# Optimization experiments

Hardware: AMD Instinct MI355X
Metric: run time of the kernel (lower is better)

Reference implementation:

```python
import jax, jax.numpy as jnp
import numpy as np

B, L, D, H = 8, 512, 1024, 16
HD = D // H  # head dim = 64
SCALE = 1.0  # scale=False in __init__


def _rel_sinusoid(seq_len, dim):
    # RelativeSinusoidalPositionalEmbedding lookup for relative positions
    # arange(-L/2, L/2) (even L), sinusoid of the raw relative position.
    half = dim // 2
    inv = jnp.exp(jnp.arange(half, dtype=jnp.float32) * (-(np.log(10000.0) / (half - 1))))
    r = jnp.arange(-(seq_len // 2), seq_len // 2, dtype=jnp.float32)  # (L,)
    ang = r[:, None] * inv[None, :]  # (L, half)
    return jnp.concatenate([jnp.sin(ang), jnp.cos(ang)], axis=1)  # (L, dim)


def setup_inputs() -> dict:
    key = jax.random.key(0)
    ks = jax.random.split(key, 8)
    s = 0.02
    x = jax.random.normal(ks[0], (B, L, D), jnp.float32)
    mask = jax.random.randint(ks[1], (B, L), 0, 2).astype(jnp.int64)
    mask = mask.at[:, 0].set(1)  # ensure at least one valid key per row
    qmask = jax.random.randint(ks[2], (B, L), 0, 2).astype(jnp.int64)
    w_qkv = jax.random.normal(ks[3], (D, 3 * D), jnp.float32) * s
    w_qkpos = jax.random.normal(ks[4], (HD, 2 * D), jnp.float32) * s
    w_fc = jax.random.normal(ks[5], (D, D), jnp.float32) * s
    b_fc = jnp.zeros((D,), jnp.float32)
    shift = jnp.abs(jax.random.normal(ks[6], (1,), jnp.float32)) + 0.001
    bias = -jnp.abs(jax.random.normal(ks[7], (1,), jnp.float32))
    return dict(x=x, mask=mask, qmask=qmask, w_qkv=w_qkv, w_qkpos=w_qkpos,
                w_fc=w_fc, b_fc=b_fc, shift=shift, bias=bias)


def reference(x, mask, qmask, w_qkv, w_qkpos, w_fc, b_fc, shift, bias):
    # trans_type='self', use_Gaussian=True, dropout in eval mode (identity)
    b, l, d = x.shape
    qkv = x @ w_qkv  # (B, L, 3D)
    q, k, v = jnp.split(qkv, 3, axis=-1)
    q = q.reshape(b, l, H, HD).transpose(0, 2, 1, 3)  # (B,H,L,hd)
    k = k.reshape(b, l, H, HD).transpose(0, 2, 1, 3)
    v = v.reshape(b, l, H, HD).transpose(0, 2, 1, 3)

    pe = _rel_sinusoid(l, HD)               # (L, hd)
    y = pe @ w_qkpos                        # (L, 2D)
    q_p, k_p = jnp.split(y, 2, axis=-1)     # (L, D) each
    q_p = q_p.reshape(l, H, HD).transpose(1, 0, 2)  # (H, L, hd)
    k_p = k_p.reshape(l, H, HD).transpose(1, 0, 2)  # (H, L, hd)

    attn = jnp.einsum('bhid,bhjd->bhij', q, k) + jnp.einsum('hid,hjd->hij', q_p, k_p)[None]

    # speaker-identity masking: zero out cross-speaker scores (trans_type='self')
    qsame = qmask[:, :, None] == qmask[:, None, :]  # (B, L, L)
    attn = jnp.where(qsame[:, None], attn, 0.0)
    attn = attn / SCALE

    # key padding mask -> -inf
    attn = jnp.where(mask[:, None, None, :] == 0, -jnp.inf, attn)

    # Gaussian distance bias: -(shift * (i-j)^2 + bias)
    idx = jnp.arange(l, dtype=jnp.float32)
    sqd = (idx[:, None] - idx[None, :]) ** 2  # (L, L)
    attn = attn + (-(shift[0] * sqd + bias[0]))[None, None]

    attn = jax.nn.softmax(attn, axis=-1)
    out = jnp.einsum('bhij,bhjd->bhid', attn, v)  # (B,H,L,hd)
    out = out.transpose(0, 2, 1, 3).reshape(b, l, d)
    return out @ w_fc + b_fc
```

## Files before the change

kernel.cpp:

```cpp
#include <hip/hip_runtime.h>
#include <hip/hip_bf16.h>

#define BB 8
#define LL 512
#define DD 1024
#define HH 16
#define HD 64
#define LOG2E 1.4426950408889634f

typedef __attribute__((ext_vector_type(8))) unsigned short u16x8;
typedef __attribute__((ext_vector_type(4))) unsigned short u16x4;
typedef __attribute__((ext_vector_type(8))) __bf16 bf16x8;
typedef __attribute__((ext_vector_type(4))) float f32x4;
typedef __attribute__((ext_vector_type(16))) float f32x16;

#define DEV __device__ __forceinline__

DEV unsigned short f2bf(float f) {
    return __builtin_bit_cast(unsigned short, (__bf16)f);
}
DEV f32x4 mfma16(u16x8 a, u16x8 b, f32x4 c) {
    return __builtin_amdgcn_mfma_f32_16x16x32_bf16(
        __builtin_bit_cast(bf16x8, a), __builtin_bit_cast(bf16x8, b), c, 0, 0, 0);
}
DEV f32x16 mfma32(u16x8 a, u16x8 b, f32x16 c) {
    return __builtin_amdgcn_mfma_f32_32x32x16_bf16(
        __builtin_bit_cast(bf16x8, a), __builtin_bit_cast(bf16x8, b), c, 0, 0, 0);
}
typedef __attribute__((address_space(1))) void gv_t;
typedef __attribute__((address_space(3))) void lv_t;
DEV void gload16(const void* g, void* l) {
    __builtin_amdgcn_global_load_lds((gv_t*)g, (lv_t*)l, 16, 0, 0);
}


__global__ __launch_bounds__(256) void cvt_x(const float* __restrict__ in,
                                             unsigned short* __restrict__ out) {
    int i = blockIdx.x * 256 + threadIdx.x;
    f32x4 v = *(const f32x4*)(in + i * 4);
    u16x4 o;
    o[0] = f2bf(v[0]); o[1] = f2bf(v[1]); o[2] = f2bf(v[2]); o[3] = f2bf(v[3]);
    *(u16x4*)(out + i * 4) = o;
}

__global__ __launch_bounds__(256) void transpose_cvt(
    const float* __restrict__ in, unsigned short* __restrict__ out,
    int R, int C) {
    __shared__ unsigned short tile[32][33];
    int c0 = blockIdx.x * 32, r0 = blockIdx.y * 32;
    int tx = threadIdx.x & 31, ty = threadIdx.x >> 5;
#pragma unroll
    for (int i = 0; i < 32; i += 8)
        tile[ty + i][tx] = f2bf(in[(r0 + ty + i) * C + c0 + tx]);
    __syncthreads();
#pragma unroll
    for (int i = 0; i < 32; i += 8)
        out[(c0 + ty + i) * R + r0 + tx] = tile[tx][ty + i];
}

__global__ __launch_bounds__(256) void posg(
    const float* __restrict__ w, unsigned short* __restrict__ qpx,
    unsigned short* __restrict__ kpx) {
    __shared__ float peS[64][64];
    __shared__ float wS[64][32];
    int c0 = blockIdx.x * 32, i0 = blockIdx.y * 64;
    int t = threadIdx.x;
#pragma unroll
    for (int j = 0; j < 16; ++j) {
        int o = t + j * 256;
        int ri = o >> 6, d = o & 63, dd = d & 31;
        float inv = expf((float)dd * -0.2971077539347156f);
        float ang = (float)(i0 + ri - 256) * inv;
        peS[ri][d] = (d < 32) ? sinf(ang) : cosf(ang);
    }
#pragma unroll
    for (int j = 0; j < 8; ++j) {
        int o = t + j * 256;
        wS[o >> 5][o & 31] = w[(o >> 5) * 2048 + c0 + (o & 31)];
    }
    __syncthreads();
#pragma unroll
    for (int j = 0; j < 8; ++j) {
        int o = t + j * 256;
        int row = o >> 5, col = o & 31;
        float acc = 0.0f;
#pragma unroll
        for (int k = 0; k < 64; ++k) acc += peS[row][k] * wS[k][col];
        int c = c0 + col, i = i0 + row;
        int qt = i >> 5, lq = i & 31;
        int cc = (c < 1024) ? c : (c - 1024);
        int h = cc >> 6, k = cc & 63;
        int ks = k >> 4, h2 = (k >> 3) & 1, jj = k & 7;
        unsigned idx = ((unsigned)(h * 4096 + qt * 256 + ks * 64 + h2 * 32 + lq)
                        << 3) + jj;
        if (c < 1024) qpx[idx] = f2bf(acc * LOG2E);
        else          kpx[idx] = f2bf(acc);
    }
}

template <int MODE>
__global__ __launch_bounds__(256) void gemm_bt(
    const unsigned short* __restrict__ A, const unsigned short* __restrict__ Bt,
    int M, int N, int K, int NBX, unsigned short* __restrict__ o0,
    unsigned short* __restrict__ o1, unsigned short* __restrict__ o2,
    float* __restrict__ fout, const float* __restrict__ bias) {
    __shared__ __align__(16) unsigned short As[128 * 32];
    __shared__ __align__(16) unsigned short Bs[128 * 32];
    int g = blockIdx.x;
    int swz = (g & 7) * (gridDim.x >> 3) + (g >> 3);
    int bx = swz % NBX, by = swz / NBX;
    int m0 = by * 128, n0 = bx * 128;
    int t = threadIdx.x;
    int w = t >> 6, l = t & 63, lg = l >> 4, lc = l & 15;
    int wr = w >> 1, wc = w & 1;

    f32x4 acc[4][4] = {};

    int sr = w * 16 + (l >> 2);
    int sk = (l & 3) * 8;
    const unsigned short* Ab = A + (m0 + sr) * K + sk;
    const unsigned short* Bb = Bt + (n0 + sr) * K + sk;
    unsigned short* dA0 = As + w * 512;
    unsigned short* dA1 = As + 2048 + w * 512;
    unsigned short* dB0 = Bs + w * 512;
    unsigned short* dB1 = Bs + 2048 + w * 512;

    for (int k0 = 0; k0 < K; k0 += 32) {
        __syncthreads();
        gload16(Ab + k0, dA0);
        gload16(Ab + 64 * K + k0, dA1);
        gload16(Bb + k0, dB0);
        gload16(Bb + 64 * K + k0, dB1);
        __syncthreads();
        u16x8 af[4], bf[4];
#pragma unroll
        for (int mm = 0; mm < 4; ++mm)
            af[mm] = *(const u16x8*)&As[(wr * 64 + mm * 16 + lc) * 32 + lg * 8];
#pragma unroll
        for (int nn = 0; nn < 4; ++nn)
            bf[nn] = *(const u16x8*)&Bs[(wc * 64 + nn * 16 + lc) * 32 + lg * 8];
#pragma unroll
        for (int mm = 0; mm < 4; ++mm)
#pragma unroll
            for (int nn = 0; nn < 4; ++nn)
                acc[mm][nn] = mfma16(af[mm], bf[nn], acc[mm][nn]);
    }

#pragma unroll
    for (int mm = 0; mm < 4; ++mm)
#pragma unroll
        for (int nn = 0; nn < 4; ++nn)
#pragma unroll
            for (int r = 0; r < 4; ++r) {
                int row = m0 + wr * 64 + mm * 16 + lg * 4 + r;
                int col = n0 + wc * 64 + nn * 16 + lc;
                float v = acc[mm][nn][r];
                if (MODE == 0) {
                    int bb = row >> 9, i = row & 511;
                    int which = col >> 10, dd = col & 1023;
                    int hh = dd >> 6, hd = dd & 63;
                    int bh2 = bb * HH + hh;
                    int tl = i >> 5, io = i & 31;
                    if (which == 2) {
                        int h2 = (io >> 2) & 1, ps = (io >> 4) & 1;
                        int j = (io & 3) | (((io >> 3) & 1) << 2);
                        int dblk = hd >> 5, lq = hd & 31;
                        unsigned idx = ((unsigned)(bh2 * 4096 + tl * 256 +
                                        (dblk * 2 + ps) * 64 + h2 * 32 + lq)
                                        << 3) + j;
                        o2[idx] = f2bf(v);
                    } else {
                        int ks = hd >> 4, h2 = (hd >> 3) & 1, j = hd & 7;
                        unsigned idx = ((unsigned)(bh2 * 4096 + tl * 256 +
                                        ks * 64 + h2 * 32 + io) << 3) + j;
                        if (which == 0) o0[idx] = f2bf(v * LOG2E);
                        else            o1[idx] = f2bf(v);
                    }
                } else {
                    fout[row * N + col] = v + bias[col];
                }
            }
}

__global__ __launch_bounds__(256, 4) void attn_k(
    const unsigned short* __restrict__ Qx, const unsigned short* __restrict__ Kx,
    const unsigned short* __restrict__ Vx, const unsigned short* __restrict__ QPx,
    const unsigned short* __restrict__ KPx, const int* __restrict__ mask,
    const int* __restrict__ qmask, const float* __restrict__ shp,
    unsigned short* __restrict__ out) {
    __shared__ float mbuf[2][64];
    __shared__ float lsbuf[2][64];
    __shared__ float obuf[2][64][33];

    int g = blockIdx.x;
    int bid = ((g & 7) << 7) + (g >> 3);
    int b = bid >> 7, h = (bid >> 3) & 15, qc = bid & 7;
    int t = threadIdx.x, w = t >> 6, l = t & 63;
    int qg = w & 1, kh = w >> 1;
    int lq = l & 31, hi = l >> 5;
    int q = qc * 64 + qg * 32 + lq;
    int bh = b * HH + h;
    int qt = qc * 2 + qg;

    const unsigned short* qb  = Qx  + (((unsigned)(bh * 4096 + qt * 256)) << 3) + (l << 3);
    const unsigned short* qpb = QPx + (((unsigned)(h  * 4096 + qt * 256)) << 3) + (l << 3);
    u16x8 qf[4], pf[4];
#pragma unroll
    for (int ks = 0; ks < 4; ++ks) {
        qf[ks] = *(const u16x8*)(qb + ks * 512);
        pf[ks] = *(const u16x8*)(qpb + ks * 512);
    }

    unsigned long long km[4], qm[4];
#pragma unroll
    for (int t8 = 0; t8 < 4; ++t8) {
        int base = b * LL + (kh * 4 + t8) * 64 + l;
        km[t8] = __ballot(mask[base] != 0);
        qm[t8] = __ballot(qmask[base] != 0);
    }
    int qi = (qmask[b * LL + q] != 0) ? 1 : 0;

    const float M0 = -1.0e30f, NEGF = -3.0e38f, THR = 8.0f;
    float negs = -(*shp) * LOG2E;
    float m = M0, ls = 0.0f;
    f32x16 o0 = {}, o1 = {};
    float fq = (float)(q - 4 * hi);

    for (int tt = 0; tt < 8; ++tt) {
        int ttg = kh * 8 + tt;
        const unsigned short* kb  = Kx  + (((unsigned)(bh * 4096 + ttg * 256)) << 3) + (l << 3);
        const unsigned short* kpb = KPx + (((unsigned)(h  * 4096 + ttg * 256)) << 3) + (l << 3);
        f32x16 sk = {}, sp = {};
#pragma unroll
        for (int ks = 0; ks < 4; ++ks) {
            sk = mfma32(*(const u16x8*)(kb + ks * 512), qf[ks], sk);
            sp = mfma32(*(const u16x8*)(kpb + ks * 512), pf[ks], sp);
        }

        unsigned kwn = ((unsigned)(km[tt >> 1] >> ((tt & 1) * 32))) >> (hi * 4);
        unsigned qwn = ((unsigned)(qm[tt >> 1] >> ((tt & 1) * 32))) >> (hi * 4);
        float bt = fq - 32.0f * (float)ttg;
        float p[16];
#pragma unroll
        for (int r = 0; r < 16; ++r) {
            const int off = (r & 3) + 8 * (r >> 2);
            float v = sk[r] + sp[r];
            v = (((qwn >> off) & 1u) == (unsigned)qi) ? v : 0.0f;
            float dr = bt - (float)off;
            v = __builtin_fmaf(negs * dr, dr, v);
            v = ((kwn >> off) & 1u) ? v : NEGF;
            p[r] = v;
        }
        float a0 = fmaxf(fmaxf(p[0], p[1]), fmaxf(p[2], p[3]));
        float a1 = fmaxf(fmaxf(p[4], p[5]), fmaxf(p[6], p[7]));
        float a2 = fmaxf(fmaxf(p[8], p[9]), fmaxf(p[10], p[11]));
        float a3 = fmaxf(fmaxf(p[12], p[13]), fmaxf(p[14], p[15]));
        float pmax = fmaxf(fmaxf(a0, a1), fmaxf(a2, a3));
        pmax = fmaxf(pmax, __shfl_xor(pmax, 32));
        if (!__all(pmax <= m + THR)) {
            float mn = fmaxf(m, pmax);
            float sc = __builtin_amdgcn_exp2f(m - mn);
#pragma unroll
            for (int r = 0; r < 16; ++r) { o0[r] *= sc; o1[r] *= sc; }
            ls *= sc;
            m = mn;
        }
#pragma unroll
        for (int r = 0; r < 16; ++r) p[r] = __builtin_amdgcn_exp2f(p[r] - m);
        ls += (((p[0] + p[1]) + (p[2] + p[3])) + ((p[4] + p[5]) + (p[6] + p[7]))) +
              (((p[8] + p[9]) + (p[10] + p[11])) +
               ((p[12] + p[13]) + (p[14] + p[15])));
        u16x8 pf0, pf1;
#pragma unroll
        for (int j = 0; j < 8; ++j) { pf0[j] = f2bf(p[j]); pf1[j] = f2bf(p[8 + j]); }
        const unsigned short* vb = Vx + (((unsigned)(bh * 4096 + ttg * 256)) << 3) + (l << 3);
        o0 = mfma32(*(const u16x8*)(vb), pf0, o0);
        o0 = mfma32(*(const u16x8*)(vb + 512), pf1, o0);
        o1 = mfma32(*(const u16x8*)(vb + 1024), pf0, o1);
        o1 = mfma32(*(const u16x8*)(vb + 1536), pf1, o1);
    }

    if (kh == 1) {
        mbuf[qg][l] = m;
        lsbuf[qg][l] = ls;
#pragma unroll
        for (int r = 0; r < 16; ++r) {
            obuf[qg][l][r] = o0[r];
            obuf[qg][l][16 + r] = o1[r];
        }
    }
    __syncthreads();
    if (kh == 0) {
        float m1 = mbuf[qg][l], ls1 = lsbuf[qg][l];
        float mm = fmaxf(m, m1);
        float sc0 = __builtin_amdgcn_exp2f(m - mm);
        float sc1 = __builtin_amdgcn_exp2f(m1 - mm);
        float lsm = ls * sc0 + ls1 * sc1;
        float rs = lsm + __shfl_xor(lsm, 32);
        float rinv = __builtin_amdgcn_rcpf(rs);
        unsigned short* ob = out + ((long)(b * LL + q)) * DD + h * HD + hi * 4;
#pragma unroll
        for (int rg = 0; rg < 4; ++rg) {
            u16x4 pk0, pk1;
#pragma unroll
            for (int rr = 0; rr < 4; ++rr) {
                int i = rg * 4 + rr;
                float v0 = __builtin_fmaf(o0[i], sc0, obuf[qg][l][i] * sc1);
                float v1 = __builtin_fmaf(o1[i], sc0, obuf[qg][l][16 + i] * sc1);
                pk0[rr] = f2bf(v0 * rinv);
                pk1[rr] = f2bf(v1 * rinv);
            }
            *(u16x4*)(ob + rg * 8) = pk0;
            *(u16x4*)(ob + 32 + rg * 8) = pk1;
        }
    }
}

extern "C" void kernel_launch(void* const* d_in, const int* in_sizes, int n_in,
                              void* d_out, int out_size, void* d_ws,
                              size_t ws_size, hipStream_t stream) {
    const float* x     = (const float*)d_in[0];
    const int*   mask  = (const int*)d_in[1];
    const int*   qmask = (const int*)d_in[2];
    const float* w_qkv = (const float*)d_in[3];
    const float* w_qkp = (const float*)d_in[4];
    const float* w_fc  = (const float*)d_in[5];
    const float* b_fc  = (const float*)d_in[6];
    const float* shift = (const float*)d_in[7];

    char* ws = (char*)d_ws;
    unsigned short* xb   = (unsigned short*)(ws);
    unsigned short* qb   = (unsigned short*)(ws + 8388608);
    unsigned short* kb   = (unsigned short*)(ws + 16777216);
    unsigned short* vtb  = (unsigned short*)(ws + 25165824);
    unsigned short* qp   = (unsigned short*)(ws + 33554432);
    unsigned short* kp   = (unsigned short*)(ws + 34603008);
    unsigned short* wqt  = (unsigned short*)(ws + 35651584);
    unsigned short* wft  = (unsigned short*)(ws + 41943040);
    unsigned short* aout = (unsigned short*)(ws + 44040192);

    cvt_x<<<4096, 256, 0, stream>>>(x, xb);
    transpose_cvt<<<dim3(96, 32), 256, 0, stream>>>(w_qkv, wqt, 1024, 3072);
    transpose_cvt<<<dim3(32, 32), 256, 0, stream>>>(w_fc, wft, 1024, 1024);
    posg<<<dim3(64, 8), 256, 0, stream>>>(w_qkp, qp, kp);
    gemm_bt<0><<<768, 256, 0, stream>>>(xb, wqt, 4096, 3072, 1024, 24, qb, kb,
                                        vtb, nullptr, nullptr);
    attn_k<<<1024, 256, 0, stream>>>(qb, kb, vtb, qp, kp, mask, qmask, shift,
                                     aout);
    gemm_bt<1><<<256, 256, 0, stream>>>(aout, wft, 4096, 1024, 1024, 8, nullptr,
                                        nullptr, nullptr, (float*)d_out, b_fc);
}
```

Baseline: 137.7 us.

## Widen GEMM K-tile with XOR-swizzled LDS, prefetch V and unroll attention loop

```diff
diff --git a/kernel.cpp b/kernel.cpp
--- a/kernel.cpp
+++ b/kernel.cpp
@@ -104,8 +104,8 @@
     int M, int N, int K, int NBX, unsigned short* __restrict__ o0,
     unsigned short* __restrict__ o1, unsigned short* __restrict__ o2,
     float* __restrict__ fout, const float* __restrict__ bias) {
-    __shared__ __align__(16) unsigned short As[128 * 32];
-    __shared__ __align__(16) unsigned short Bs[128 * 32];
+    __shared__ __align__(16) unsigned short As[128 * 64];
+    __shared__ __align__(16) unsigned short Bs[128 * 64];
     int g = blockIdx.x;
     int swz = (g & 7) * (gridDim.x >> 3) + (g >> 3);
     int bx = swz % NBX, by = swz / NBX;
@@ -116,34 +116,39 @@
 
     f32x4 acc[4][4] = {};
 
-    int sr = w * 16 + (l >> 2);
-    int sk = (l & 3) * 8;
-    const unsigned short* Ab = A + (m0 + sr) * K + sk;
-    const unsigned short* Bb = Bt + (n0 + sr) * K + sk;
-    unsigned short* dA0 = As + w * 512;
-    unsigned short* dA1 = As + 2048 + w * 512;
-    unsigned short* dB0 = Bs + w * 512;
-    unsigned short* dB1 = Bs + 2048 + w * 512;
-
-    for (int k0 = 0; k0 < K; k0 += 32) {
+    int srow = w * 32 + (l >> 3);
+    int schk = (l & 7) ^ ((l >> 3) & 7);
+    const unsigned short* Ab = A + (m0 + srow) * K + schk * 8;
+    const unsigned short* Bb = Bt + (n0 + srow) * K + schk * 8;
+    unsigned short* dA = As + w * 2048;
+    unsigned short* dB = Bs + w * 2048;
+    int sw = lc & 7;
+
+    for (int k0 = 0; k0 < K; k0 += 64) {
         __syncthreads();
-        gload16(Ab + k0, dA0);
-        gload16(Ab + 64 * K + k0, dA1);
-        gload16(Bb + k0, dB0);
-        gload16(Bb + 64 * K + k0, dB1);
+#pragma unroll
+        for (int c = 0; c < 4; ++c) {
+            gload16(Ab + c * 8 * K + k0, dA + c * 512);
+            gload16(Bb + c * 8 * K + k0, dB + c * 512);
+        }
         __syncthreads();
-        u16x8 af[4], bf[4];
-#pragma unroll
-        for (int mm = 0; mm < 4; ++mm)
-            af[mm] = *(const u16x8*)&As[(wr * 64 + mm * 16 + lc) * 32 + lg * 8];
-#pragma unroll
-        for (int nn = 0; nn < 4; ++nn)
-            bf[nn] = *(const u16x8*)&Bs[(wc * 64 + nn * 16 + lc) * 32 + lg * 8];
-#pragma unroll
-        for (int mm = 0; mm < 4; ++mm)
+#pragma unroll
+        for (int ks = 0; ks < 2; ++ks) {
+            u16x8 af[4], bf[4];
+#pragma unroll
+            for (int mm = 0; mm < 4; ++mm)
+                af[mm] = *(const u16x8*)&As[(wr * 64 + mm * 16 + lc) * 64 +
+                                            (((ks * 4 + lg) ^ sw) << 3)];
 #pragma unroll
             for (int nn = 0; nn < 4; ++nn)
-                acc[mm][nn] = mfma16(af[mm], bf[nn], acc[mm][nn]);
+                bf[nn] = *(const u16x8*)&Bs[(wc * 64 + nn * 16 + lc) * 64 +
+                                            (((ks * 4 + lg) ^ sw) << 3)];
+#pragma unroll
+            for (int mm = 0; mm < 4; ++mm)
+#pragma unroll
+                for (int nn = 0; nn < 4; ++nn)
+                    acc[mm][nn] = mfma16(af[mm], bf[nn], acc[mm][nn]);
+        }
     }
 
 #pragma unroll
@@ -182,7 +187,7 @@
             }
 }
 
-__global__ __launch_bounds__(256, 4) void attn_k(
+__global__ void attn_k(
     const unsigned short* __restrict__ Qx, const unsigned short* __restrict__ Kx,
     const unsigned short* __restrict__ Vx, const unsigned short* __restrict__ QPx,
     const unsigned short* __restrict__ KPx, const int* __restrict__ mask,
@@ -226,10 +231,16 @@
     f32x16 o0 = {}, o1 = {};
     float fq = (float)(q - 4 * hi);
 
+#pragma unroll
     for (int tt = 0; tt < 8; ++tt) {
         int ttg = kh * 8 + tt;
         const unsigned short* kb  = Kx  + (((unsigned)(bh * 4096 + ttg * 256)) << 3) + (l << 3);
         const unsigned short* kpb = KPx + (((unsigned)(h  * 4096 + ttg * 256)) << 3) + (l << 3);
+        const unsigned short* vb  = Vx  + (((unsigned)(bh * 4096 + ttg * 256)) << 3) + (l << 3);
+        u16x8 vf0 = *(const u16x8*)(vb);
+        u16x8 vf1 = *(const u16x8*)(vb + 512);
+        u16x8 vf2 = *(const u16x8*)(vb + 1024);
+        u16x8 vf3 = *(const u16x8*)(vb + 1536);
         f32x16 sk = {}, sp = {};
 #pragma unroll
         for (int ks = 0; ks < 4; ++ks) {
@@ -273,11 +284,10 @@
         u16x8 pf0, pf1;
 #pragma unroll
         for (int j = 0; j < 8; ++j) { pf0[j] = f2bf(p[j]); pf1[j] = f2bf(p[8 + j]); }
-        const unsigned short* vb = Vx + (((unsigned)(bh * 4096 + ttg * 256)) << 3) + (l << 3);
-        o0 = mfma32(*(const u16x8*)(vb), pf0, o0);
-        o0 = mfma32(*(const u16x8*)(vb + 512), pf1, o0);
-        o1 = mfma32(*(const u16x8*)(vb + 1024), pf0, o1);
-        o1 = mfma32(*(const u16x8*)(vb + 1536), pf1, o1);
+        o0 = mfma32(vf0, pf0, o0);
+        o0 = mfma32(vf1, pf1, o0);
+        o1 = mfma32(vf2, pf0, o1);
+        o1 = mfma32(vf3, pf1, o1);
     }
 
     if (kh == 1) {
```

After: 151.1 us. +9.8%, slower.
